# Kernel optimization log

Hardware: AMD Instinct MI355X
Metric: run time of the kernel (lower is better)

Reference implementation:

```python
import jax, jax.numpy as jnp
import numpy as np

DIM = 1024
H = 16
HEAD_DIM = 64
HIDDEN = H * HEAD_DIM  # == DIM, required by the module's reshape
SCALE = HEAD_DIM ** -0.5


def setup_inputs() -> dict:
    key = jax.random.key(0)
    k_x, k_qkv, k_w1, k_b1 = jax.random.split(key, 4)
    B, N = 8, 1024
    x = jax.random.normal(k_x, (B, N, DIM), dtype=jnp.float32)
    # nn.Linear stores weight as [out, in]; we keep [in, out] for x @ W
    w_qkv = jax.random.normal(k_qkv, (DIM, 3 * HIDDEN), dtype=jnp.float32) * (DIM ** -0.5)
    w_out = jax.random.normal(k_w1, (HIDDEN, DIM), dtype=jnp.float32) * (HIDDEN ** -0.5)
    b_out = jax.random.normal(k_b1, (DIM,), dtype=jnp.float32) * 0.02
    return {"x": x, "w_qkv": w_qkv, "w_out": w_out, "b_out": b_out}


def reference(x, w_qkv, w_out, b_out):
    B, N, C = x.shape
    # QKV projection (no bias), split into heads
    qkv = (x @ w_qkv).reshape(B, N, 3, H, C // H)
    q, k, v = qkv[:, :, 0], qkv[:, :, 1], qkv[:, :, 2]  # [B, N, H, d]
    attn = jnp.einsum("bqhd,bkhd->bhqk", q, k) * SCALE
    attn = jax.nn.softmax(attn, axis=-1)  # dropout inactive at eval
    out = jnp.einsum("bhqk,bkhd->bqhd", attn, v).reshape(B, N, C)
    return out @ w_out + b_out
```

## Files before the change

### kernel.cpp

```cpp
#include <hip/hip_runtime.h>
#include <hip/hip_bf16.h>

#define B_SZ 8
#define SEQ 1024
#define DIM_ 1024
#define NH 16
#define HD 64
#define M_TOT (B_SZ*SEQ)
#define N_QKV (3*DIM_)

typedef __attribute__((ext_vector_type(8))) short bf16x8;
typedef __attribute__((ext_vector_type(4))) float f32x4;

typedef const __attribute__((address_space(1))) void gvoid;
typedef __attribute__((address_space(3))) void lvoid;

__device__ __forceinline__ short f2bf(float f){
  union { __hip_bfloat16 h; short s; } u;
  u.h = __float2bfloat16(f);
  return u.s;
}

__global__ void cvt_kernel(const float* __restrict__ in, short* __restrict__ out, int n4){
  int i = blockIdx.x*blockDim.x + threadIdx.x;
  int stride = gridDim.x*blockDim.x;
  for (; i < n4; i += stride){
    float4 v = reinterpret_cast<const float4*>(in)[i];
    short4 s;
    s.x = f2bf(v.x); s.y = f2bf(v.y); s.z = f2bf(v.z); s.w = f2bf(v.w);
    reinterpret_cast<short4*>(out)[i] = s;
  }
}

__global__ void tconv_kernel(const float* __restrict__ in, short* __restrict__ out, int R, int C){
  __shared__ alignas(16) short tile[64][66];
  const int l = threadIdx.x & 63, w = threadIdx.x >> 6;
  const int r0 = blockIdx.y * 64, c0 = blockIdx.x * 64;
  #pragma unroll
  for (int rr = 0; rr < 16; ++rr){
    int r = w + rr*4;
    tile[r][l] = f2bf(in[(size_t)(r0+r)*C + c0 + l]);
  }
  __syncthreads();
  #pragma unroll
  for (int cc = 0; cc < 16; ++cc){
    int c = w + cc*4;
    out[(size_t)(c0+c)*R + r0 + l] = tile[l][c];
  }
}

template<int EPI, int GX, int NOFF>
__global__ __launch_bounds__(256, 4) void gemm5(
    const short* __restrict__ A, const short* __restrict__ Bt,
    int M, int Nn, int K,
    short* __restrict__ Qb, short* __restrict__ Kb, short* __restrict__ Vtb,
    const float* __restrict__ bias, float* __restrict__ outF)
{
  __shared__ alignas(16) short As[2][128*32];
  __shared__ alignas(16) short Bs[2][128*32];

  const int orig = blockIdx.x;
  const int xcd = orig & 7, t = orig >> 3;
  const int by = xcd*8 + t/GX, bx = t % GX;

  const int tid = threadIdx.x;
  const int l = tid & 63, wid = tid >> 6;
  const int wr = wid >> 1, wc = wid & 1;
  const int lr = l & 15, lw = l >> 4;
  const int sw = (lr >> 1) & 3;
  const int m0 = by * 128, n0 = (bx + NOFF) * 128;

  f32x4 acc[4][4];
  const f32x4 zz = {0.f,0.f,0.f,0.f};
  #pragma unroll
  for (int m=0;m<4;m++)
    #pragma unroll
    for (int n=0;n<4;n++) acc[m][n] = zz;

  auto STAGE = [&](int buf, int kt){
    const int k0 = kt << 5;
    #pragma unroll
    for (int j=0;j<2;j++){
      const int idx = j*256 + tid;
      const int row = idx >> 2;
      const int ws  = (idx & 3) ^ ((row >> 1) & 3);
      __builtin_amdgcn_global_load_lds(
          (gvoid*)(A + (size_t)(m0+row)*K + k0 + ws*8),
          (lvoid*)(&As[buf][idx*8]), 16, 0, 0);
    }
    #pragma unroll
    for (int j=0;j<2;j++){
      const int idx = j*256 + tid;
      const int row = idx >> 2;
      const int ws  = (idx & 3) ^ ((row >> 1) & 3);
      __builtin_amdgcn_global_load_lds(
          (gvoid*)(Bt + (size_t)(n0+row)*K + k0 + ws*8),
          (lvoid*)(&Bs[buf][idx*8]), 16, 0, 0);
    }
  };

  STAGE(0, 0);
  __syncthreads();

  const int NT = K >> 5;
  int buf = 0;
  for (int kt = 0; kt < NT; ++kt){
    if (kt + 1 < NT) STAGE(buf ^ 1, kt + 1);

    bf16x8 af[4], bfr[4];
    const int wsel = (lw ^ sw) << 3;
    #pragma unroll
    for (int m=0;m<4;m++){
      const int r = wr*64 + m*16 + lr;
      af[m] = *(const bf16x8*)(&As[buf][r*32 + wsel]);
    }
    #pragma unroll
    for (int n=0;n<4;n++){
      const int r = wc*64 + n*16 + lr;
      bfr[n] = *(const bf16x8*)(&Bs[buf][r*32 + wsel]);
    }
    #pragma unroll
    for (int m=0;m<4;m++)
      #pragma unroll
      for (int n=0;n<4;n++)
        acc[m][n] = __builtin_amdgcn_mfma_f32_16x16x32_bf16(af[m], bfr[n], acc[m][n], 0, 0, 0);

    __syncthreads();
    buf ^= 1;
  }

  #pragma unroll
  for (int n=0;n<4;n++){
    const int col = n0 + wc*64 + n*16 + lr;
    if (EPI == 0){
      const int three = col >> 10;
      const int cc = col & 1023;
      const int h = cc >> 6, d = cc & 63;
      #pragma unroll
      for (int m=0;m<4;m++){
        const int rbase = m0 + wr*64 + m*16 + (lw<<2);
        const int b = rbase >> 10, nn = rbase & 1023;
        const int bh = b*NH + h;
        if (three == 2){
          short4 pk;
          pk.x = f2bf(acc[m][n][0]); pk.y = f2bf(acc[m][n][1]);
          pk.z = f2bf(acc[m][n][2]); pk.w = f2bf(acc[m][n][3]);
          *(short4*)(&Vtb[((size_t)bh*HD + d)*SEQ + nn]) = pk;
        } else if (three == 0){
          #pragma unroll
          for (int ri=0;ri<4;ri++)
            Qb[((size_t)bh*SEQ + nn + ri)*HD + d] = f2bf(acc[m][n][ri] * 0.1803368801f);
        } else {
          #pragma unroll
          for (int ri=0;ri<4;ri++)
            Kb[((size_t)bh*SEQ + nn + ri)*HD + d] = f2bf(acc[m][n][ri]);
        }
      }
    } else {
      const float bv = bias[col];
      #pragma unroll
      for (int m=0;m<4;m++){
        const int rbase = m0 + wr*64 + m*16 + (lw<<2);
        #pragma unroll
        for (int ri=0;ri<4;ri++)
          outF[(size_t)(rbase+ri)*Nn + col] = acc[m][n][ri] + bv;
      }
    }
  }
}

__global__ __launch_bounds__(256) void attn_kernel(
    const short* __restrict__ Q, const short* __restrict__ Kb,
    const short* __restrict__ Vt, short* __restrict__ Ao)
{
  __shared__ alignas(16) short Ks[2][64*64];
  __shared__ alignas(16) short Vs[2][64*64];
  __shared__ alignas(16) short Ps[4][16*72];

  const int tid = threadIdx.x;
  const int l = tid & 63, w = tid >> 6;
  const int bid = blockIdx.x;
  const int qt = bid & 15, bh = bid >> 4;
  const int b = bh >> 4, h = bh & 15;
  const size_t base = (size_t)bh << 16;

  const int lr = l & 15;
  const int q4 = l >> 4;
  const int lk = q4 << 3;
  const int sw8 = lr & 7;

  const int qrow = qt*64 + w*16 + lr;
  const short* qp = Q + base + (size_t)qrow*HD + lk;
  const bf16x8 qf0 = *(const bf16x8*)qp;
  const bf16x8 qf1 = *(const bf16x8*)(qp + 32);

  float l_run = 0.f;
  f32x4 o[4];
  #pragma unroll
  for (int i=0;i<4;i++) o[i] = f32x4{0.f,0.f,0.f,0.f};

  bf16x8 kr[2], vr[2];
  auto load_tile = [&](int kt){
    const int kv0 = kt*64;
    #pragma unroll
    for (int p=0;p<2;p++){
      const int idx = tid + p*256;
      const int row = idx >> 3, c8 = (idx & 7) << 3;
      kr[p] = *(const bf16x8*)(Kb + base + (size_t)(kv0+row)*HD + c8);
      vr[p] = *(const bf16x8*)(Vt + base + (size_t)row*SEQ + kv0 + c8);
    }
  };
  auto write_tile = [&](int bi){
    #pragma unroll
    for (int p=0;p<2;p++){
      const int idx = tid + p*256;
      const int row = idx >> 3;
      const int wsw = ((idx & 7) ^ (row & 7)) << 3;
      *(bf16x8*)(&Ks[bi][row*64 + wsw]) = kr[p];
      *(bf16x8*)(&Vs[bi][row*64 + wsw]) = vr[p];
    }
  };

  load_tile(0);
  write_tile(0);
  __syncthreads();

  int cur = 0;
  for (int kt = 0; kt < 16; ++kt){
    if (kt < 15) load_tile(kt+1);

    const short* kb = &Ks[cur][0];
    const short* vb = &Vs[cur][0];

    f32x4 s[4];
    #pragma unroll
    for (int cg=0;cg<4;cg++) s[cg] = f32x4{0.f,0.f,0.f,0.f};
    __builtin_amdgcn_s_setprio(1);
    #pragma unroll
    for (int cg=0;cg<4;cg++){
      const short* kp = kb + (cg*16 + lr)*64;
      bf16x8 kf0 = *(const bf16x8*)(kp + ((q4     ^ sw8) << 3));
      bf16x8 kf1 = *(const bf16x8*)(kp + (((q4+4) ^ sw8) << 3));
      s[cg] = __builtin_amdgcn_mfma_f32_16x16x32_bf16(kf0, qf0, s[cg], 0,0,0);
      s[cg] = __builtin_amdgcn_mfma_f32_16x16x32_bf16(kf1, qf1, s[cg], 0,0,0);
    }
    __builtin_amdgcn_s_setprio(0);

    float rs = 0.f;
    short* pw = &Ps[w][0];
    #pragma unroll
    for (int cg=0;cg<4;cg++){
      float p0 = __builtin_amdgcn_exp2f(s[cg][0]);
      float p1 = __builtin_amdgcn_exp2f(s[cg][1]);
      float p2 = __builtin_amdgcn_exp2f(s[cg][2]);
      float p3 = __builtin_amdgcn_exp2f(s[cg][3]);
      rs += (p0+p1)+(p2+p3);
      short4 pk; pk.x=f2bf(p0); pk.y=f2bf(p1); pk.z=f2bf(p2); pk.w=f2bf(p3);
      *(short4*)(pw + lr*72 + cg*16 + q4*4) = pk;
    }
    rs += __shfl_xor(rs, 16);
    rs += __shfl_xor(rs, 32);
    l_run += rs;

    const bf16x8 pa0 = *(const bf16x8*)(pw + lr*72 + lk);
    const bf16x8 pa1 = *(const bf16x8*)(pw + lr*72 + lk + 32);
    __builtin_amdgcn_s_setprio(1);
    #pragma unroll
    for (int dg=0;dg<4;dg++){
      const short* vp = vb + (dg*16 + lr)*64;
      bf16x8 vf0 = *(const bf16x8*)(vp + ((q4     ^ sw8) << 3));
      bf16x8 vf1 = *(const bf16x8*)(vp + (((q4+4) ^ sw8) << 3));
      o[dg] = __builtin_amdgcn_mfma_f32_16x16x32_bf16(pa0, vf0, o[dg], 0,0,0);
      o[dg] = __builtin_amdgcn_mfma_f32_16x16x32_bf16(pa1, vf1, o[dg], 0,0,0);
    }
    __builtin_amdgcn_s_setprio(0);

    if (kt < 15) write_tile(cur ^ 1);
    __syncthreads();
    cur ^= 1;
  }

  float linv[4];
  #pragma unroll
  for (int ri=0;ri<4;ri++) linv[ri] = 1.0f / __shfl(l_run, (q4<<2) + ri);
  #pragma unroll
  for (int ri=0;ri<4;ri++){
    const int row = qt*64 + w*16 + (q4<<2) + ri;
    short* op = Ao + ((size_t)(b*SEQ + row))*DIM_ + h*HD;
    #pragma unroll
    for (int dg=0;dg<4;dg++)
      op[dg*16 + lr] = f2bf(o[dg][ri] * linv[ri]);
  }
}

extern "C" void kernel_launch(void* const* d_in, const int* in_sizes, int n_in,
                              void* d_out, int out_size, void* d_ws, size_t ws_size,
                              hipStream_t stream)
{
  (void)in_sizes; (void)n_in; (void)out_size; (void)ws_size;
  const float* x     = (const float*)d_in[0];
  const float* w_qkv = (const float*)d_in[1];
  const float* w_out = (const float*)d_in[2];
  const float* b_out = (const float*)d_in[3];
  float* out = (float*)d_out;

  char* ws = (char*)d_ws;
  const size_t MB = (size_t)1 << 20;
  short* xb    = (short*)(ws);
  short* wqkvT = (short*)(ws + 16*MB);
  short* woutT = (short*)(ws + 22*MB);
  short* Qb    = (short*)(ws + 24*MB);
  short* Kb    = (short*)(ws + 40*MB);
  short* Vtb   = (short*)(ws + 56*MB);
  short* Aob   = (short*)(ws + 72*MB);

  cvt_kernel<<<2048, 256, 0, stream>>>(x, xb, (M_TOT*DIM_)/4);
  tconv_kernel<<<dim3(N_QKV/64, DIM_/64), 256, 0, stream>>>(w_qkv, wqkvT, DIM_, N_QKV);
  tconv_kernel<<<dim3(DIM_/64, DIM_/64), 256, 0, stream>>>(w_out, woutT, DIM_, DIM_);

  gemm5<0,16,0><<<1024, 256, 0, stream>>>(
      xb, wqkvT, M_TOT, N_QKV, DIM_, Qb, Kb, Vtb, nullptr, nullptr);

  gemm5<0,8,16><<<512, 256, 0, stream>>>(
      xb, wqkvT, M_TOT, N_QKV, DIM_, Qb, Kb, Vtb, nullptr, nullptr);

  attn_kernel<<<B_SZ*NH*(SEQ/64), 256, 0, stream>>>(Qb, Kb, Vtb, Aob);

  gemm5<1,8,0><<<512, 256, 0, stream>>>(
      Aob, woutT, M_TOT, DIM_, DIM_, nullptr, nullptr, nullptr, b_out, out);
}
```

Before: 180.1 us.

## Process 128 query rows per attention block and remap blocks per XCD; merge QKV GEMM launches

The attention kernel now has each wave handle two 16-row query groups (128 query rows per block), so every K/V tile loaded into shared memory feeds twice as many MFMAs and the block count halves to 1024. Block IDs are remapped so that blocks sharing a batch-head land on the same XCD, improving L2 reuse of K/V. The two QKV projection GEMM launches are merged into a single launch with a 24-wide column range. The cost is doubled accumulator registers per wave, which may reduce occupancy, and fewer blocks for load balancing.

```diff
diff --git a/kernel.cpp b/kernel.cpp
--- a/kernel.cpp
+++ b/kernel.cpp
@@ -175,12 +175,14 @@
 {
   __shared__ alignas(16) short Ks[2][64*64];
   __shared__ alignas(16) short Vs[2][64*64];
-  __shared__ alignas(16) short Ps[4][16*72];
+  __shared__ alignas(16) short Ps[4][32*72];
 
   const int tid = threadIdx.x;
   const int l = tid & 63, w = tid >> 6;
-  const int bid = blockIdx.x;
-  const int qt = bid & 15, bh = bid >> 4;
+  const int orig = blockIdx.x;
+  const int xcd = orig & 7, n_ = orig >> 3;
+  const int g = n_ >> 3, qt = n_ & 7;
+  const int bh = g*8 + xcd;
   const int b = bh >> 4, h = bh & 15;
   const size_t base = (size_t)bh << 16;
 
@@ -189,15 +191,18 @@
   const int lk = q4 << 3;
   const int sw8 = lr & 7;
 
-  const int qrow = qt*64 + w*16 + lr;
-  const short* qp = Q + base + (size_t)qrow*HD + lk;
-  const bf16x8 qf0 = *(const bf16x8*)qp;
-  const bf16x8 qf1 = *(const bf16x8*)(qp + 32);
-
-  float l_run = 0.f;
-  f32x4 o[4];
-  #pragma unroll
-  for (int i=0;i<4;i++) o[i] = f32x4{0.f,0.f,0.f,0.f};
+  const int qrowA = qt*128 + w*32 + lr;
+  const short* qpA = Q + base + (size_t)qrowA*HD + lk;
+  const bf16x8 qfA0 = *(const bf16x8*)qpA;
+  const bf16x8 qfA1 = *(const bf16x8*)(qpA + 32);
+  const short* qpB = qpA + 16*HD;
+  const bf16x8 qfB0 = *(const bf16x8*)qpB;
+  const bf16x8 qfB1 = *(const bf16x8*)(qpB + 32);
+
+  float lA = 0.f, lB = 0.f;
+  f32x4 oA[4], oB[4];
+  #pragma unroll
+  for (int i=0;i<4;i++){ oA[i] = f32x4{0.f,0.f,0.f,0.f}; oB[i] = f32x4{0.f,0.f,0.f,0.f}; }
 
   bf16x8 kr[2], vr[2];
   auto load_tile = [&](int kt){
@@ -232,46 +237,59 @@
     const short* kb = &Ks[cur][0];
     const short* vb = &Vs[cur][0];
 
-    f32x4 s[4];
-    #pragma unroll
-    for (int cg=0;cg<4;cg++) s[cg] = f32x4{0.f,0.f,0.f,0.f};
+    f32x4 sA[4], sB[4];
+    #pragma unroll
+    for (int cg=0;cg<4;cg++){ sA[cg] = f32x4{0.f,0.f,0.f,0.f}; sB[cg] = f32x4{0.f,0.f,0.f,0.f}; }
     __builtin_amdgcn_s_setprio(1);
     #pragma unroll
     for (int cg=0;cg<4;cg++){
       const short* kp = kb + (cg*16 + lr)*64;
       bf16x8 kf0 = *(const bf16x8*)(kp + ((q4     ^ sw8) << 3));
       bf16x8 kf1 = *(const bf16x8*)(kp + (((q4+4) ^ sw8) << 3));
-      s[cg] = __builtin_amdgcn_mfma_f32_16x16x32_bf16(kf0, qf0, s[cg], 0,0,0);
-      s[cg] = __builtin_amdgcn_mfma_f32_16x16x32_bf16(kf1, qf1, s[cg], 0,0,0);
+      sA[cg] = __builtin_amdgcn_mfma_f32_16x16x32_bf16(kf0, qfA0, sA[cg], 0,0,0);
+      sA[cg] = __builtin_amdgcn_mfma_f32_16x16x32_bf16(kf1, qfA1, sA[cg], 0,0,0);
+      sB[cg] = __builtin_amdgcn_mfma_f32_16x16x32_bf16(kf0, qfB0, sB[cg], 0,0,0);
+      sB[cg] = __builtin_amdgcn_mfma_f32_16x16x32_bf16(kf1, qfB1, sB[cg], 0,0,0);
     }
     __builtin_amdgcn_s_setprio(0);
 
-    float rs = 0.f;
     short* pw = &Ps[w][0];
+    float rsA = 0.f, rsB = 0.f;
     #pragma unroll
     for (int cg=0;cg<4;cg++){
-      float p0 = __builtin_amdgcn_exp2f(s[cg][0]);
-      float p1 = __builtin_amdgcn_exp2f(s[cg][1]);
-      float p2 = __builtin_amdgcn_exp2f(s[cg][2]);
-      float p3 = __builtin_amdgcn_exp2f(s[cg][3]);
-      rs += (p0+p1)+(p2+p3);
-      short4 pk; pk.x=f2bf(p0); pk.y=f2bf(p1); pk.z=f2bf(p2); pk.w=f2bf(p3);
-      *(short4*)(pw + lr*72 + cg*16 + q4*4) = pk;
-    }
-    rs += __shfl_xor(rs, 16);
-    rs += __shfl_xor(rs, 32);
-    l_run += rs;
-
-    const bf16x8 pa0 = *(const bf16x8*)(pw + lr*72 + lk);
-    const bf16x8 pa1 = *(const bf16x8*)(pw + lr*72 + lk + 32);
+      float a0 = __builtin_amdgcn_exp2f(sA[cg][0]);
+      float a1 = __builtin_amdgcn_exp2f(sA[cg][1]);
+      float a2 = __builtin_amdgcn_exp2f(sA[cg][2]);
+      float a3 = __builtin_amdgcn_exp2f(sA[cg][3]);
+      rsA += (a0+a1)+(a2+a3);
+      short4 ka; ka.x=f2bf(a0); ka.y=f2bf(a1); ka.z=f2bf(a2); ka.w=f2bf(a3);
+      *(short4*)(pw + lr*72 + cg*16 + q4*4) = ka;
+      float b0 = __builtin_amdgcn_exp2f(sB[cg][0]);
+      float b1 = __builtin_amdgcn_exp2f(sB[cg][1]);
+      float b2 = __builtin_amdgcn_exp2f(sB[cg][2]);
+      float b3 = __builtin_amdgcn_exp2f(sB[cg][3]);
+      rsB += (b0+b1)+(b2+b3);
+      short4 kb_; kb_.x=f2bf(b0); kb_.y=f2bf(b1); kb_.z=f2bf(b2); kb_.w=f2bf(b3);
+      *(short4*)(pw + (16+lr)*72 + cg*16 + q4*4) = kb_;
+    }
+    rsA += __shfl_xor(rsA, 16); rsA += __shfl_xor(rsA, 32); lA += rsA;
+    rsB += __shfl_xor(rsB, 16); rsB += __shfl_xor(rsB, 32); lB += rsB;
+
+    const bf16x8 paA0 = *(const bf16x8*)(pw + lr*72 + lk);
+    const bf16x8 paA1 = *(const bf16x8*)(pw + lr*72 + lk + 32);
+    const bf16x8 paB0 = *(const bf16x8*)(pw + (16+lr)*72 + lk);
+    const bf16x8 paB1 = *(const bf16x8*)(pw + (16+lr)*72 + lk + 32);
+
     __builtin_amdgcn_s_setprio(1);
     #pragma unroll
     for (int dg=0;dg<4;dg++){
       const short* vp = vb + (dg*16 + lr)*64;
       bf16x8 vf0 = *(const bf16x8*)(vp + ((q4     ^ sw8) << 3));
       bf16x8 vf1 = *(const bf16x8*)(vp + (((q4+4) ^ sw8) << 3));
-      o[dg] = __builtin_amdgcn_mfma_f32_16x16x32_bf16(pa0, vf0, o[dg], 0,0,0);
-      o[dg] = __builtin_amdgcn_mfma_f32_16x16x32_bf16(pa1, vf1, o[dg], 0,0,0);
+      oA[dg] = __builtin_amdgcn_mfma_f32_16x16x32_bf16(paA0, vf0, oA[dg], 0,0,0);
+      oA[dg] = __builtin_amdgcn_mfma_f32_16x16x32_bf16(paA1, vf1, oA[dg], 0,0,0);
+      oB[dg] = __builtin_amdgcn_mfma_f32_16x16x32_bf16(paB0, vf0, oB[dg], 0,0,0);
+      oB[dg] = __builtin_amdgcn_mfma_f32_16x16x32_bf16(paB1, vf1, oB[dg], 0,0,0);
     }
     __builtin_amdgcn_s_setprio(0);
 
@@ -280,16 +298,22 @@
     cur ^= 1;
   }
 
-  float linv[4];
-  #pragma unroll
-  for (int ri=0;ri<4;ri++) linv[ri] = 1.0f / __shfl(l_run, (q4<<2) + ri);
+  float linvA[4], linvB[4];
   #pragma unroll
   for (int ri=0;ri<4;ri++){
-    const int row = qt*64 + w*16 + (q4<<2) + ri;
-    short* op = Ao + ((size_t)(b*SEQ + row))*DIM_ + h*HD;
-    #pragma unroll
-    for (int dg=0;dg<4;dg++)
-      op[dg*16 + lr] = f2bf(o[dg][ri] * linv[ri]);
+    linvA[ri] = 1.0f / __shfl(lA, (q4<<2) + ri);
+    linvB[ri] = 1.0f / __shfl(lB, (q4<<2) + ri);
+  }
+  #pragma unroll
+  for (int ri=0;ri<4;ri++){
+    const int rowA = qt*128 + w*32 + (q4<<2) + ri;
+    short* opA = Ao + ((size_t)(b*SEQ + rowA))*DIM_ + h*HD;
+    short* opB = opA + 16*DIM_;
+    #pragma unroll
+    for (int dg=0;dg<4;dg++){
+      opA[dg*16 + lr] = f2bf(oA[dg][ri] * linvA[ri]);
+      opB[dg*16 + lr] = f2bf(oB[dg][ri] * linvB[ri]);
+    }
   }
 }
 
@@ -318,13 +342,10 @@
   tconv_kernel<<<dim3(N_QKV/64, DIM_/64), 256, 0, stream>>>(w_qkv, wqkvT, DIM_, N_QKV);
   tconv_kernel<<<dim3(DIM_/64, DIM_/64), 256, 0, stream>>>(w_out, woutT, DIM_, DIM_);
 
-  gemm5<0,16,0><<<1024, 256, 0, stream>>>(
+  gemm5<0,24,0><<<1536, 256, 0, stream>>>(
       xb, wqkvT, M_TOT, N_QKV, DIM_, Qb, Kb, Vtb, nullptr, nullptr);
 
-  gemm5<0,8,16><<<512, 256, 0, stream>>>(
-      xb, wqkvT, M_TOT, N_QKV, DIM_, Qb, Kb, Vtb, nullptr, nullptr);
-
-  attn_kernel<<<B_SZ*NH*(SEQ/64), 256, 0, stream>>>(Qb, Kb, Vtb, Aob);
+  attn_kernel<<<1024, 256, 0, stream>>>(Qb, Kb, Vtb, Aob);
 
   gemm5<1,8,0><<<512, 256, 0, stream>>>(
       Aob, woutT, M_TOT, DIM_, DIM_, nullptr, nullptr, nullptr, b_out, out);
```

After: 167.5 us. -7.0%, faster.
